# Kernel tuning notes

Measured on AMD Instinct MI355X. Metric: run time of the kernel, lower is better.

Reference implementation:

```python
import jax, jax.numpy as jnp
import numpy as np

# Uniform 3-level taxonomy: 128 roots, branching 16 then 16.
N0, B1, B2 = 128, 16, 16
N1, N2 = N0 * B1, N0 * B1 * B2          # 2048, 32768
TOTAL = N0 + N1 + N2                    # 34944
BATCH = 1024
W = (1.0, 1.0, 1.0)                     # level_weights
NEG = -100000000.0                      # fill value used by the torch module


def _ce(logits, tgt):
    # per-sample cross entropy, reduction='none': logits [B,C], tgt [B] -> [B]
    return -jnp.take_along_axis(jax.nn.log_softmax(logits, axis=-1), tgt[:, None], axis=1)[:, 0]


def setup_inputs() -> dict:
    key = jax.random.key(0)
    k1, k2, k3, k4 = jax.random.split(key, 4)
    outputs = jax.random.normal(k1, (BATCH, TOTAL), dtype=jnp.float32)
    # hierarchically consistent labels (relative-within-level ids, as labelmap expects)
    r0 = jax.random.randint(k2, (BATCH,), 0, N0, dtype=jnp.int32)
    r1 = jax.random.randint(k3, (BATCH,), 0, B1, dtype=jnp.int32)
    r2 = jax.random.randint(k4, (BATCH,), 0, B2, dtype=jnp.int32)
    lab1 = r0 * B1 + r1
    lab2 = lab1 * B2 + r2
    level_labels = jnp.stack([r0, lab1, lab2], axis=1)  # [B, 3] int32
    return {"outputs": outputs, "level_labels": level_labels}


def reference(outputs, level_labels):
    lab0, lab1, lab2 = level_labels[:, 0], level_labels[:, 1], level_labels[:, 2]
    r1 = lab1 - lab0 * B1   # new_level_labels[1]: label relative to true parent's children
    r2 = lab2 - lab1 * B2   # new_level_labels[2]

    out0 = outputs[:, :N0]                 # [B, N0]
    out1 = outputs[:, N0:N0 + N1]          # [B, N1]
    out2 = outputs[:, N0 + N1:]            # [B, N2]

    # ---- level 0: possible children == all roots, so masked CE == full CE
    loss0 = _ce(out0, lab0)
    pred0 = jnp.argmax(out0, axis=1).astype(jnp.int32)          # predicted root (relative)
    found0 = pred0 != lab0                                      # found_incorrect after level 0

    # ---- level 1
    g1_true = jnp.take_along_axis(out1.reshape(BATCH, N0, B1), lab0[:, None, None], axis=1)[:, 0, :]
    loss1 = jnp.where(found0, _ce(out1, lab1), _ce(g1_true, r1))
    g1_pred = jnp.take_along_axis(out1.reshape(BATCH, N0, B1), pred0[:, None, None], axis=1)[:, 0, :]
    pred1_in = jnp.argmax(g1_pred, axis=1).astype(jnp.int32)    # argmax within predicted parent's children
    pred1 = pred0 * B1 + pred1_in                               # predicted level-1 class (relative)
    found1 = found0 | (pred1_in != r1)

    # ---- level 2
    g2_true = jnp.take_along_axis(out2.reshape(BATCH, N1, B2), lab1[:, None, None], axis=1)[:, 0, :]
    loss2 = jnp.where(found1, _ce(out2, lab2), _ce(g2_true, r2))

    # ---- outputs_new: level-0 slice fully copied; levels 1/2 only children of the predicted path
    mask1 = (jnp.arange(N1, dtype=jnp.int32) // B1)[None, :] == pred0[:, None]
    mask2 = (jnp.arange(N2, dtype=jnp.int32) // B2)[None, :] == pred1[:, None]
    outputs_new = jnp.concatenate(
        [out0, jnp.where(mask1, out1, NEG), jnp.where(mask2, out2, NEG)], axis=1)

    # torch accumulates size-1 tensors; torch.mean of the final [1] tensor == total sum
    loss = jnp.sum(W[0] * loss0 + W[1] * loss1 + W[2] * loss2)
    return outputs_new, loss
```

## Files before the change

### kernel.cpp

```cpp
#include <hip/hip_runtime.h>
#include <math.h>

#define N0v 128
#define B1v 16
#define B2v 16
#define N1v 2048
#define N2v 32768
#define TOTALv 34944
#define BATCHv 1024
#define NEGV -100000000.0f

typedef __attribute__((ext_vector_type(4))) float f32x4;

__global__ __launch_bounds__(1024, 8) void row_kernel(
    const float* __restrict__ outs, const int* __restrict__ labels,
    float* __restrict__ out, float* __restrict__ partials)
{
    const int b   = blockIdx.x;
    const int tid = threadIdx.x;
    const int wid = tid >> 6, lane = tid & 63;
    const float* rowp = outs + (size_t)b * TOTALv;
    float*       orow = out  + (size_t)b * TOTALv;
    const f32x4* rv4 = reinterpret_cast<const f32x4*>(rowp);
    f32x4*       ov4 = reinterpret_cast<f32x4*>(orow);
    const f32x4  neg4 = {NEGV, NEGV, NEGV, NEGV};

    __shared__ float sm_gsum[128];
    __shared__ int   sm_gidx[128];
    __shared__ float s_wmax[2]; __shared__ int s_wmi[2];
    __shared__ float s_red[16][3];
    __shared__ int   s_i[2];
    __shared__ float s_loss[2];

    const int lab0 = labels[b * 3 + 0];
    const int lab1 = labels[b * 3 + 1];
    const int lab2 = labels[b * 3 + 2];

    float v0 = 0.f;
    if (tid < N0v) v0 = rowp[tid];
    f32x4 a = {0.f, 0.f, 0.f, 0.f};
    if (tid < 512) a = rv4[32 + tid];
    const f32x4* b2 = rv4 + 544;
    f32x4*       o2 = ov4 + 544;
    f32x4 cur = b2[tid];
    float eg2 = 0.f;
    if (tid < 16) eg2 = rowp[N0v + N1v + lab1 * B2v + tid];
    float t0 = 0.f, t1 = 0.f, t2 = 0.f;
    if (tid == 0) { t0 = rowp[lab0]; t1 = rowp[N0v + lab1]; t2 = rowp[N0v + N1v + lab2]; }
    __builtin_amdgcn_sched_barrier(0);

    float s1 = 0.f;
    if (tid < 512) {
        s1 = __expf(a.x) + __expf(a.y) + __expf(a.z) + __expf(a.w);
        float gm = a.x; int gi = 0;
        if (a.y > gm) { gm = a.y; gi = 1; }
        if (a.z > gm) { gm = a.z; gi = 2; }
        if (a.w > gm) { gm = a.w; gi = 3; }
        gi += (tid & 3) * 4;
        float gs = s1;
        float ov = __shfl_xor(gm, 1); int oi = __shfl_xor(gi, 1);
        gs += __shfl_xor(gs, 1);
        if (ov > gm || (ov == gm && oi < gi)) { gm = ov; gi = oi; }
        ov = __shfl_xor(gm, 2); oi = __shfl_xor(gi, 2);
        gs += __shfl_xor(gs, 2);
        if (ov > gm || (ov == gm && oi < gi)) { gm = ov; gi = oi; }
        if ((tid & 3) == 0) { sm_gsum[tid >> 2] = gs; sm_gidx[tid >> 2] = gi; }
    }

    if (tid < N0v) {
        float mv = v0; int mi = tid;
        #pragma unroll
        for (int off = 32; off; off >>= 1) {
            float ovv = __shfl_down(mv, off);
            int   oii = __shfl_down(mi, off);
            if (ovv > mv || (ovv == mv && oii < mi)) { mv = ovv; mi = oii; }
        }
        if (lane == 0) { s_wmax[wid] = mv; s_wmi[wid] = mi; }
    }

    if (tid < 16) {
        eg2 = __expf(eg2);
        #pragma unroll
        for (int off = 8; off; off >>= 1) eg2 += __shfl_xor(eg2, off);
    }

    float r0 = (tid < N0v) ? __expf(v0) : 0.f;
    #pragma unroll
    for (int off = 32; off; off >>= 1) {
        r0 += __shfl_down(r0, off);
        s1 += __shfl_down(s1, off);
    }
    if (lane == 0) { s_red[wid][0] = r0; s_red[wid][1] = s1; }

    __syncthreads();

    if (tid == 0) {
        float m0 = s_wmax[0]; int p0 = s_wmi[0];
        if (s_wmax[1] > m0 || (s_wmax[1] == m0 && s_wmi[1] < p0)) { m0 = s_wmax[1]; p0 = s_wmi[1]; }
        const int p1i = sm_gidx[p0];
        s_i[0] = p0; s_i[1] = p1i;
        float S0 = 0.f, S1 = 0.f;
        #pragma unroll
        for (int w = 0; w < 16; ++w) { S0 += s_red[w][0]; S1 += s_red[w][1]; }
        const float Sg1 = sm_gsum[lab0];
        const int r1 = lab1 - lab0 * B1v;
        const bool found0 = (p0 != lab0);
        const bool found1 = found0 || (p1i != r1);
        const float loss0 = __logf(S0) - t0;
        const float loss1 = (found0 ? __logf(S1) : __logf(Sg1)) - t1;
        s_loss[0] = loss0 + loss1 - t2 + (found1 ? 0.f : __logf(eg2));
        s_loss[1] = found1 ? 1.f : 0.f;
    }

    __syncthreads();
    const int pred0 = s_i[0];
    const int pred1 = pred0 * B1v + s_i[1];

    if (tid < 512) {
        __builtin_nontemporal_store(((tid >> 2) == pred0) ? a : neg4, &ov4[32 + tid]);
        if (tid < N0v) __builtin_nontemporal_store(v0, &orow[tid]);
    }

    float s2 = 0.f;
    int idx = tid;
    #pragma unroll
    for (int it = 0; it < 7; ++it) {
        const f32x4 nxt = b2[idx + 1024];
        s2 += __expf(cur.x) + __expf(cur.y) + __expf(cur.z) + __expf(cur.w);
        __builtin_nontemporal_store(((idx >> 2) == pred1) ? cur : neg4, &o2[idx]);
        cur = nxt; idx += 1024;
    }
    s2 += __expf(cur.x) + __expf(cur.y) + __expf(cur.z) + __expf(cur.w);
    __builtin_nontemporal_store(((idx >> 2) == pred1) ? cur : neg4, &o2[idx]);

    #pragma unroll
    for (int off = 32; off; off >>= 1) s2 += __shfl_down(s2, off);
    if (lane == 0) s_red[wid][2] = s2;
    __syncthreads();
    if (tid == 0) {
        float S2 = 0.f;
        #pragma unroll
        for (int w = 0; w < 16; ++w) S2 += s_red[w][2];
        partials[b] = s_loss[0] + s_loss[1] * __logf(S2);
    }
}

__global__ __launch_bounds__(256) void loss_reduce(
    const float* __restrict__ partials, float* __restrict__ out_loss)
{
    __shared__ float sh[4];
    const int tid = threadIdx.x;
    float s = 0.f;
    for (int i = tid; i < BATCHv; i += 256) s += partials[i];
    #pragma unroll
    for (int off = 32; off; off >>= 1) s += __shfl_down(s, off);
    if ((tid & 63) == 0) sh[tid >> 6] = s;
    __syncthreads();
    if (tid == 0) *out_loss = sh[0] + sh[1] + sh[2] + sh[3];
}

extern "C" void kernel_launch(void* const* d_in, const int* in_sizes, int n_in,
                              void* d_out, int out_size, void* d_ws, size_t ws_size,
                              hipStream_t stream) {
    const float* outs   = (const float*)d_in[0];
    const int*   labels = (const int*)d_in[1];
    float*       out    = (float*)d_out;
    float*       part   = (float*)d_ws;

    row_kernel<<<BATCHv, 1024, 0, stream>>>(outs, labels, out, part);
    loss_reduce<<<1, 256, 0, stream>>>(part, out + (size_t)BATCHv * TOTALv);
}
```

Before: 50.71 us.

## Pre-fill masked output with NEG early and patch predicted children after

The kernel now writes NEG to all level-1 and level-2 output slots at the start, before any reduction, and computes the level-2 exp-sum before the first barrier. This merges the separate second reduction and barrier into the first one. After the predicted path is known, only the 16 predicted children at each level are overwritten with the real values, re-read from the input. The intent is to remove the second __syncthreads and the dependency of the bulk stores on the argmax, so writes overlap with compute. The cost is that the predicted slots are written twice, and the write-after-write to the same addresses relies on the stores staying ordered.

```diff
diff --git a/kernel.cpp b/kernel.cpp
--- a/kernel.cpp
+++ b/kernel.cpp
@@ -30,7 +30,6 @@
     __shared__ float s_wmax[2]; __shared__ int s_wmi[2];
     __shared__ float s_red[16][3];
     __shared__ int   s_i[2];
-    __shared__ float s_loss[2];
 
     const int lab0 = labels[b * 3 + 0];
     const int lab1 = labels[b * 3 + 1];
@@ -47,7 +46,11 @@
     if (tid < 16) eg2 = rowp[N0v + N1v + lab1 * B2v + tid];
     float t0 = 0.f, t1 = 0.f, t2 = 0.f;
     if (tid == 0) { t0 = rowp[lab0]; t1 = rowp[N0v + lab1]; t2 = rowp[N0v + N1v + lab2]; }
-    __builtin_amdgcn_sched_barrier(0);
+
+    if (tid < 512) __builtin_nontemporal_store(neg4, &ov4[32 + tid]);
+    #pragma unroll
+    for (int k = 0; k < 8; ++k)
+        __builtin_nontemporal_store(neg4, &o2[tid + 1024 * k]);
 
     float s1 = 0.f;
     if (tid < 512) {
@@ -68,6 +71,7 @@
     }
 
     if (tid < N0v) {
+        __builtin_nontemporal_store(v0, &orow[tid]);
         float mv = v0; int mi = tid;
         #pragma unroll
         for (int off = 32; off; off >>= 1) {
@@ -84,13 +88,26 @@
         for (int off = 8; off; off >>= 1) eg2 += __shfl_xor(eg2, off);
     }
 
+    float s2 = 0.f;
+    {
+        int idx = tid;
+        #pragma unroll
+        for (int it = 0; it < 7; ++it) {
+            const f32x4 nxt = b2[idx + 1024];
+            s2 += __expf(cur.x) + __expf(cur.y) + __expf(cur.z) + __expf(cur.w);
+            cur = nxt; idx += 1024;
+        }
+        s2 += __expf(cur.x) + __expf(cur.y) + __expf(cur.z) + __expf(cur.w);
+    }
+
     float r0 = (tid < N0v) ? __expf(v0) : 0.f;
     #pragma unroll
     for (int off = 32; off; off >>= 1) {
         r0 += __shfl_down(r0, off);
         s1 += __shfl_down(s1, off);
+        s2 += __shfl_down(s2, off);
     }
-    if (lane == 0) { s_red[wid][0] = r0; s_red[wid][1] = s1; }
+    if (lane == 0) { s_red[wid][0] = r0; s_red[wid][1] = s1; s_red[wid][2] = s2; }
 
     __syncthreads();
 
@@ -99,49 +116,28 @@
         if (s_wmax[1] > m0 || (s_wmax[1] == m0 && s_wmi[1] < p0)) { m0 = s_wmax[1]; p0 = s_wmi[1]; }
         const int p1i = sm_gidx[p0];
         s_i[0] = p0; s_i[1] = p1i;
-        float S0 = 0.f, S1 = 0.f;
+        float S0 = 0.f, S1 = 0.f, S2 = 0.f;
         #pragma unroll
-        for (int w = 0; w < 16; ++w) { S0 += s_red[w][0]; S1 += s_red[w][1]; }
+        for (int w = 0; w < 16; ++w) { S0 += s_red[w][0]; S1 += s_red[w][1]; S2 += s_red[w][2]; }
         const float Sg1 = sm_gsum[lab0];
         const int r1 = lab1 - lab0 * B1v;
         const bool found0 = (p0 != lab0);
         const bool found1 = found0 || (p1i != r1);
         const float loss0 = __logf(S0) - t0;
         const float loss1 = (found0 ? __logf(S1) : __logf(Sg1)) - t1;
-        s_loss[0] = loss0 + loss1 - t2 + (found1 ? 0.f : __logf(eg2));
-        s_loss[1] = found1 ? 1.f : 0.f;
+        const float loss2 = (found1 ? __logf(S2) : __logf(eg2)) - t2;
+        partials[b] = loss0 + loss1 + loss2;
     }
 
     __syncthreads();
     const int pred0 = s_i[0];
     const int pred1 = pred0 * B1v + s_i[1];
 
-    if (tid < 512) {
-        __builtin_nontemporal_store(((tid >> 2) == pred0) ? a : neg4, &ov4[32 + tid]);
-        if (tid < N0v) __builtin_nontemporal_store(v0, &orow[tid]);
-    }
-
-    float s2 = 0.f;
-    int idx = tid;
-    #pragma unroll
-    for (int it = 0; it < 7; ++it) {
-        const f32x4 nxt = b2[idx + 1024];
-        s2 += __expf(cur.x) + __expf(cur.y) + __expf(cur.z) + __expf(cur.w);
-        __builtin_nontemporal_store(((idx >> 2) == pred1) ? cur : neg4, &o2[idx]);
-        cur = nxt; idx += 1024;
-    }
-    s2 += __expf(cur.x) + __expf(cur.y) + __expf(cur.z) + __expf(cur.w);
-    __builtin_nontemporal_store(((idx >> 2) == pred1) ? cur : neg4, &o2[idx]);
-
-    #pragma unroll
-    for (int off = 32; off; off >>= 1) s2 += __shfl_down(s2, off);
-    if (lane == 0) s_red[wid][2] = s2;
-    __syncthreads();
-    if (tid == 0) {
-        float S2 = 0.f;
-        #pragma unroll
-        for (int w = 0; w < 16; ++w) S2 += s_red[w][2];
-        partials[b] = s_loss[0] + s_loss[1] * __logf(S2);
+    if (tid < 512 && (tid >> 2) == pred0)
+        __builtin_nontemporal_store(a, &ov4[32 + tid]);
+    if (tid < 4) {
+        const f32x4 g = b2[pred1 * 4 + tid];
+        __builtin_nontemporal_store(g, &o2[pred1 * 4 + tid]);
     }
 }
 
```

Result: slower. 52.09 us (+2.7%).

## Use inline-asm nontemporal stores and fold loss reduction into atomicAdd

Applied to the files above, without the earlier changes.

Replaces the compiler nontemporal store builtins with inline global_store_dwordx4/dword carrying sc0 sc1 nt cache bits, so the streaming output bypasses the caches. It also drops the separate loss_reduce kernel: each row block atomically adds its partial loss into the output scalar, which is zeroed by a memset. This trades a kernel launch for a memset plus 1024 float atomics, making the summation order nondeterministic. A trailing s_waitcnt makes sure the asm stores finish before the kernel exits.

```diff
diff --git a/kernel.cpp b/kernel.cpp
--- a/kernel.cpp
+++ b/kernel.cpp
@@ -12,9 +12,16 @@
 
 typedef __attribute__((ext_vector_type(4))) float f32x4;
 
+__device__ __forceinline__ void nt_store4(f32x4 v, f32x4* p) {
+    asm volatile("global_store_dwordx4 %0, %1, off sc0 sc1 nt" :: "v"(p), "v"(v));
+}
+__device__ __forceinline__ void nt_store1(float v, float* p) {
+    asm volatile("global_store_dword %0, %1, off sc0 sc1 nt" :: "v"(p), "v"(v));
+}
+
 __global__ __launch_bounds__(1024, 8) void row_kernel(
     const float* __restrict__ outs, const int* __restrict__ labels,
-    float* __restrict__ out, float* __restrict__ partials)
+    float* __restrict__ out, float* __restrict__ loss_out)
 {
     const int b   = blockIdx.x;
     const int tid = threadIdx.x;
@@ -117,8 +124,8 @@
     const int pred1 = pred0 * B1v + s_i[1];
 
     if (tid < 512) {
-        __builtin_nontemporal_store(((tid >> 2) == pred0) ? a : neg4, &ov4[32 + tid]);
-        if (tid < N0v) __builtin_nontemporal_store(v0, &orow[tid]);
+        nt_store4(((tid >> 2) == pred0) ? a : neg4, &ov4[32 + tid]);
+        if (tid < N0v) nt_store1(v0, &orow[tid]);
     }
 
     float s2 = 0.f;
@@ -127,11 +134,11 @@
     for (int it = 0; it < 7; ++it) {
         const f32x4 nxt = b2[idx + 1024];
         s2 += __expf(cur.x) + __expf(cur.y) + __expf(cur.z) + __expf(cur.w);
-        __builtin_nontemporal_store(((idx >> 2) == pred1) ? cur : neg4, &o2[idx]);
+        nt_store4(((idx >> 2) == pred1) ? cur : neg4, &o2[idx]);
         cur = nxt; idx += 1024;
     }
     s2 += __expf(cur.x) + __expf(cur.y) + __expf(cur.z) + __expf(cur.w);
-    __builtin_nontemporal_store(((idx >> 2) == pred1) ? cur : neg4, &o2[idx]);
+    nt_store4(((idx >> 2) == pred1) ? cur : neg4, &o2[idx]);
 
     #pragma unroll
     for (int off = 32; off; off >>= 1) s2 += __shfl_down(s2, off);
@@ -141,22 +148,10 @@
         float S2 = 0.f;
         #pragma unroll
         for (int w = 0; w < 16; ++w) S2 += s_red[w][2];
-        partials[b] = s_loss[0] + s_loss[1] * __logf(S2);
+        atomicAdd(loss_out, s_loss[0] + s_loss[1] * __logf(S2));
     }
-}
 
-__global__ __launch_bounds__(256) void loss_reduce(
-    const float* __restrict__ partials, float* __restrict__ out_loss)
-{
-    __shared__ float sh[4];
-    const int tid = threadIdx.x;
-    float s = 0.f;
-    for (int i = tid; i < BATCHv; i += 256) s += partials[i];
-    #pragma unroll
-    for (int off = 32; off; off >>= 1) s += __shfl_down(s, off);
-    if ((tid & 63) == 0) sh[tid >> 6] = s;
-    __syncthreads();
-    if (tid == 0) *out_loss = sh[0] + sh[1] + sh[2] + sh[3];
+    asm volatile("s_waitcnt vmcnt(0)" ::: "memory");
 }
 
 extern "C" void kernel_launch(void* const* d_in, const int* in_sizes, int n_in,
@@ -165,8 +160,8 @@
     const float* outs   = (const float*)d_in[0];
     const int*   labels = (const int*)d_in[1];
     float*       out    = (float*)d_out;
-    float*       part   = (float*)d_ws;
+    float*       loss   = out + (size_t)BATCHv * TOTALv;
 
-    row_kernel<<<BATCHv, 1024, 0, stream>>>(outs, labels, out, part);
-    loss_reduce<<<1, 256, 0, stream>>>(part, out + (size_t)BATCHv * TOTALv);
+    hipMemsetAsync((void*)loss, 0, sizeof(float), stream);
+    row_kernel<<<BATCHv, 1024, 0, stream>>>(outs, labels, out, loss);
 }
```

Result: slower. 53.24 us (+5.0%).
